# Performance work log

Hardware: AMD Instinct MI355X
Metric: run time of the kernel (lower is better)

## Reference

```python
import jax, jax.numpy as jnp
import numpy as np

B, L, IN, OUT = 32, 2048, 192, 2
H, N2, NL = 512, 32, 4  # hidden_dim, d_state//2 complex modes, num_layers


def setup_inputs() -> dict:
    key = jax.random.key(0)
    ks = jax.random.split(key, 8)
    neural_input = jax.random.normal(ks[0], (B, L, IN), jnp.float32)
    W_in = jax.random.normal(ks[1], (IN, H), jnp.float32) / np.sqrt(IN)
    b_in = jnp.zeros((H,), jnp.float32)
    # S4D kernel params (stacked over layers)
    log_dt = jax.random.uniform(ks[2], (NL, H), jnp.float32, np.log(1e-3), np.log(1e-1))
    Cri = jax.random.normal(ks[3], (NL, H, N2, 2), jnp.float32)  # complex C as (re, im)
    log_A_real = jnp.full((NL, H, N2), np.log(0.5), jnp.float32)
    A_imag = jnp.broadcast_to(np.pi * jnp.arange(N2, dtype=np.float32), (NL, H, N2)).astype(jnp.float32)
    D = jax.random.normal(ks[4], (NL, H), jnp.float32)
    # position-wise output conv1x1 producing 2H channels for GLU
    conv_w = jax.random.normal(ks[5], (NL, 2 * H, H), jnp.float32) / np.sqrt(H)
    conv_b = jnp.zeros((NL, 2 * H), jnp.float32)
    W_out = jax.random.normal(ks[6], (H, OUT), jnp.float32) / np.sqrt(H)
    b_out = jnp.zeros((OUT,), jnp.float32)
    return dict(neural_input=neural_input, W_in=W_in, b_in=b_in, log_dt=log_dt,
                Cri=Cri, log_A_real=log_A_real, A_imag=A_imag, D=D,
                conv_w=conv_w, conv_b=conv_b, W_out=W_out, b_out=b_out)


def _s4d_layer(u, log_dt, Cri, log_A_real, A_imag, D, conv_w, conv_b):
    # u: (B, H, L)
    Lx = u.shape[-1]
    dt = jnp.exp(log_dt)[:, None]                       # (H, 1)
    C = Cri[..., 0] + 1j * Cri[..., 1]                  # (H, N2) complex
    A = -jnp.exp(log_A_real) + 1j * A_imag              # (H, N2)
    dtA = A * dt                                        # (H, N2)
    Ct = C * (jnp.exp(dtA) - 1.0) / A                   # (H, N2)
    # Vandermonde kernel: K[h, l] = 2 Re sum_n Ct[h,n] exp(dtA[h,n] * l)
    vand = jnp.exp(dtA[..., None] * jnp.arange(Lx))     # (H, N2, L) complex
    K = 2.0 * jnp.einsum('hn,hnl->hl', Ct, vand).real   # (H, L)
    # circular conv via FFT at length 2L (== linear conv, causal)
    k_f = jnp.fft.rfft(K, n=2 * Lx)
    u_f = jnp.fft.rfft(u, n=2 * Lx)
    y = jnp.fft.irfft(u_f * k_f, n=2 * Lx)[..., :Lx]    # (B, H, L)
    y = y + u * D[:, None]
    y = jax.nn.gelu(y, approximate=False)               # torch nn.GELU (erf)
    # conv1x1 to 2H channels + GLU over channel dim
    z = jnp.einsum('oh,bhl->bol', conv_w, y) + conv_b[None, :, None]
    a, b = jnp.split(z, 2, axis=1)
    return a * jax.nn.sigmoid(b)


def reference(neural_input, W_in, b_in, log_dt, Cri, log_A_real, A_imag, D,
              conv_w, conv_b, W_out, b_out):
    x = neural_input @ W_in + b_in          # (B, L, H)
    u = jnp.transpose(x, (0, 2, 1))         # (B, H, L) channels-first for SSM
    for i in range(NL):
        u = _s4d_layer(u, log_dt[i], Cri[i], log_A_real[i], A_imag[i],
                       D[i], conv_w[i], conv_b[i])
    y = jnp.transpose(u, (0, 2, 1))         # (B, L, H)
    return y @ W_out + b_out                # (B, L, OUT)
```

## Files before the change

kernel.cpp:

```cpp
#include <hip/hip_runtime.h>
#include <hip/hip_bf16.h>
#include <math.h>

#define BB 32
#define LL 2048
#define INP 192
#define OUTC 2
#define HH 512
#define NN2 32
#define NNL 4
#define TABB 32768

using short8 = __attribute__((ext_vector_type(8))) short;
using f32x4  = __attribute__((ext_vector_type(4))) float;
using f32x2  = __attribute__((ext_vector_type(2))) float;

__device__ __forceinline__ float sigmoidf_(float x) {
  return 1.0f / (1.0f + expf(-x));
}
__device__ __forceinline__ unsigned short bf16bits(float x) {
  __hip_bfloat16 b = __float2bfloat16(x);
  return __builtin_bit_cast(unsigned short, b);
}
__device__ __forceinline__ float bfval(unsigned short b) {
  unsigned int u = (unsigned int)b << 16;
  return __builtin_bit_cast(float, u);
}
__device__ __forceinline__ float gelu_fast(float x) {
  float s = x * 0.70710678118654752f;
  float ax = fabsf(s);
  float tt = 1.0f / fmaf(0.3275911f, ax, 1.0f);
  float p = fmaf(1.061405429f, tt, -1.453152027f);
  p = fmaf(p, tt, 1.421413741f);
  p = fmaf(p, tt, -0.284496736f);
  p = fmaf(p, tt, 0.254829592f);
  float e = __expf(-s * s);
  float er = 1.0f - p * tt * e;
  er = copysignf(er, s);
  return 0.5f * x * (1.0f + er);
}
__device__ __forceinline__ void gload16(const void* gsrc, void* ldst) {
  __builtin_amdgcn_global_load_lds(
      (const __attribute__((address_space(1))) void*)gsrc,
      (__attribute__((address_space(3))) void*)ldst, 16, 0, 0);
}

__global__ __launch_bounds__(256) void k_params(const float* __restrict__ log_dt,
                                                const float* __restrict__ Cri,
                                                const float* __restrict__ lAr,
                                                const float* __restrict__ Aim,
                                                float* __restrict__ P) {
  int idx = blockIdx.x * 256 + threadIdx.x;
  if (idx >= NNL * HH * NN2) return;
  float dt  = expf(log_dt[idx / NN2]);
  float Are = -expf(lAr[idx]);
  float Aimv = Aim[idx];
  float dre = Are * dt, dim = Aimv * dt;
  float er = expf(dre);
  float wrv = er * cosf(dim);
  float wiv = er * sinf(dim);
  float Er = wrv - 1.0f, Ei = wiv;
  float den = Are * Are + Aimv * Aimv;
  float Fr = (Er * Are + Ei * Aimv) / den;
  float Fi = (Ei * Are - Er * Aimv) / den;
  float Cre = Cri[idx * 2 + 0], Cim = Cri[idx * 2 + 1];
  P[idx * 4 + 0] = wrv;
  P[idx * 4 + 1] = wiv;
  P[idx * 4 + 2] = 2.0f * (Cre * Fr - Cim * Fi);
  P[idx * 4 + 3] = 2.0f * (Cre * Fi + Cim * Fr);
}

__global__ __launch_bounds__(64) void k_tables(const float* __restrict__ P,
                                               char* __restrict__ Tab) {
  __shared__ float kk[32];
  int tid = threadIdx.x;
  int lh = blockIdx.x;
  char* tb = Tab + (size_t)lh * TABB;
  if (tid < 32) {
    int n = tid;
    const float4 pq = reinterpret_cast<const float4*>(P)[(size_t)lh * NN2 + n];
    float wr = pq.x, wi = pq.y, c2r = pq.z, c2i = pq.w;
    int mt = n >> 4;
    float pr = 1.0f, pi = 0.0f;
    for (int d = 0; d < 32; ++d) {
      {
        int t_ = 31 - d;
        int lane = ((t_ >> 3) << 4) + (n & 15);
        int j = t_ & 7;
        unsigned short hr = bf16bits(pr);
        unsigned short lr = bf16bits(pr - bfval(hr));
        unsigned short hi_ = bf16bits(pi);
        unsigned short li_ = bf16bits(pi - bfval(hi_));
        *(unsigned short*)(tb + (mt * 2 + 0) * 1024 + lane * 16 + j * 2) = hr;
        *(unsigned short*)(tb + (mt * 2 + 1) * 1024 + lane * 16 + j * 2) = hi_;
        *(unsigned short*)(tb + 4096 + (mt * 2 + 0) * 1024 + lane * 16 + j * 2) = lr;
        *(unsigned short*)(tb + 4096 + (mt * 2 + 1) * 1024 + lane * 16 + j * 2) = li_;
      }
      {
        int mtT = d >> 4;
        int lane = (((n & 15) >> 2) << 4) + (d & 15);
        int jre = n & 3, jim = (n & 3) + 4;
        unsigned short hr = bf16bits(pr);
        unsigned short lr = bf16bits(pr - bfval(hr));
        float nim = -pi;
        unsigned short hi_ = bf16bits(nim);
        unsigned short li_ = bf16bits(nim - bfval(hi_));
        char* bh = tb + 8192 + (mtT * 2 + mt) * 1024 + lane * 16;
        char* bl = tb + 12288 + (mtT * 2 + mt) * 1024 + lane * 16;
        *(unsigned short*)(bh + jre * 2) = hr;
        *(unsigned short*)(bh + jim * 2) = hi_;
        *(unsigned short*)(bl + jre * 2) = lr;
        *(unsigned short*)(bl + jim * 2) = li_;
      }
      float kp = c2r * pr - c2i * pi;
      #pragma unroll
      for (int k = 1; k < 32; k <<= 1) kp += __shfl_xor(kp, k, 32);
      if (n == 0) kk[d] = kp;
      float nr = pr * wr - pi * wi;
      pi = pr * wi + pi * wr;
      pr = nr;
    }
    float w32r = pr, w32i = pi;
    float c2wr = c2r * wr - c2i * wi;
    float c2wi = c2r * wi + c2i * wr;
    int s = ((n >> 4) << 2) + (n & 3);
    int gg = (n & 15) >> 2;
    float pmr = 1.0f, pmi = 0.0f;
    for (int m = 0; m < 16; ++m) {
      float* q = (float*)(tb + 20480 + (size_t)((s * 64) + (gg * 16 + m)) * 24);
      q[0] = w32r; q[1] = w32i; q[2] = pmr; q[3] = pmi; q[4] = c2wr; q[5] = c2wi;
      float t2 = pmr * w32r - pmi * w32i;
      pmi = pmr * w32i + pmi * w32r;
      pmr = t2;
    }
  }
  __syncthreads();
  for (int idx = tid; idx < 1024; idx += 64) {
    int mt = idx >> 9, rem = idx & 511;
    int lane = rem >> 3, j = rem & 7;
    int tt = (mt << 4) + (lane & 15);
    int jf = ((lane >> 4) << 3) + j;
    float val = (jf <= tt) ? kk[tt - jf] : 0.0f;
    unsigned short hb = bf16bits(val);
    unsigned short lb = bf16bits(val - bfval(hb));
    *(unsigned short*)(tb + 16384 + mt * 1024 + lane * 16 + j * 2) = hb;
    *(unsigned short*)(tb + 18432 + mt * 1024 + lane * 16 + j * 2) = lb;
  }
}

__global__ __launch_bounds__(256) void k_tobf16(const float* __restrict__ src,
                                                __hip_bfloat16* __restrict__ dst,
                                                int n) {
  int i = (blockIdx.x * 256 + threadIdx.x) * 4;
  if (i >= n) return;
  float4 v = *reinterpret_cast<const float4*>(&src[i]);
  dst[i + 0] = __float2bfloat16(v.x);
  dst[i + 1] = __float2bfloat16(v.y);
  dst[i + 2] = __float2bfloat16(v.z);
  dst[i + 3] = __float2bfloat16(v.w);
}

__global__ __launch_bounds__(256) void k_splitx(const float* __restrict__ src,
                                                __hip_bfloat16* __restrict__ hi,
                                                __hip_bfloat16* __restrict__ lo,
                                                int n) {
  int i = (blockIdx.x * 256 + threadIdx.x) * 4;
  if (i >= n) return;
  float4 v = *reinterpret_cast<const float4*>(&src[i]);
  float vv[4] = {v.x, v.y, v.z, v.w};
  unsigned short hb[4], lb[4];
  #pragma unroll
  for (int j = 0; j < 4; ++j) {
    hb[j] = bf16bits(vv[j]);
    lb[j] = bf16bits(vv[j] - bfval(hb[j]));
  }
  *reinterpret_cast<uint2*>(hi + i) = make_uint2(
      (unsigned)hb[0] | ((unsigned)hb[1] << 16), (unsigned)hb[2] | ((unsigned)hb[3] << 16));
  *reinterpret_cast<uint2*>(lo + i) = make_uint2(
      (unsigned)lb[0] | ((unsigned)lb[1] << 16), (unsigned)lb[2] | ((unsigned)lb[3] << 16));
}

__global__ __launch_bounds__(256) void k_prepwt(const float* __restrict__ W,
                                                __hip_bfloat16* __restrict__ hi,
                                                __hip_bfloat16* __restrict__ lo) {
  int idx = blockIdx.x * 256 + threadIdx.x;
  if (idx >= HH * INP) return;
  int h = idx / INP, k = idx - h * INP;
  float v = W[(size_t)k * HH + h];
  unsigned short hb = bf16bits(v);
  hi[idx] = __builtin_bit_cast(__hip_bfloat16, hb);
  lo[idx] = __float2bfloat16(v - bfval(hb));
}

__global__ __launch_bounds__(256) void k_ingemm(const __hip_bfloat16* __restrict__ Xhi,
                                                const __hip_bfloat16* __restrict__ Xlo,
                                                const __hip_bfloat16* __restrict__ Wthi,
                                                const __hip_bfloat16* __restrict__ Wtlo,
                                                const float* __restrict__ bias,
                                                float* __restrict__ U) {
  int lt = blockIdx.x * 128;
  int ht = blockIdx.y * 128;
  int b  = blockIdx.z;
  int t = threadIdx.x;
  int wid = t >> 6, lane = t & 63;
  int wrow = wid >> 1, wcol = wid & 1;
  int l15 = lane & 15, g = lane >> 4;

  const short* Xh = (const short*)Xhi + (size_t)b * LL * INP;
  const short* Xl = (const short*)Xlo + (size_t)b * LL * INP;
  const short* Bh = (const short*)Wthi;
  const short* Bl = (const short*)Wtlo;

  f32x4 acc[4][4];
  #pragma unroll
  for (int m = 0; m < 4; ++m)
    #pragma unroll
    for (int n = 0; n < 4; ++n) acc[m][n] = f32x4{0.f, 0.f, 0.f, 0.f};

  int lbase = lt + wrow * 64 + l15;
  int hbase = ht + wcol * 64 + l15;

  #pragma unroll
  for (int ks = 0; ks < 6; ++ks) {
    int k0 = ks * 32 + 8 * g;
    short8 ah[4], al[4], bh[4], bl[4];
    #pragma unroll
    for (int m = 0; m < 4; ++m) {
      size_t off = (size_t)(lbase + m * 16) * INP + k0;
      ah[m] = *reinterpret_cast<const short8*>(Xh + off);
      al[m] = *reinterpret_cast<const short8*>(Xl + off);
    }
    #pragma unroll
    for (int n = 0; n < 4; ++n) {
      size_t off = (size_t)(hbase + n * 16) * INP + k0;
      bh[n] = *reinterpret_cast<const short8*>(Bh + off);
      bl[n] = *reinterpret_cast<const short8*>(Bl + off);
    }
    #pragma unroll
    for (int m = 0; m < 4; ++m)
      #pragma unroll
      for (int n = 0; n < 4; ++n) {
        acc[m][n] = __builtin_amdgcn_mfma_f32_16x16x32_bf16(ah[m], bh[n], acc[m][n], 0, 0, 0);
        acc[m][n] = __builtin_amdgcn_mfma_f32_16x16x32_bf16(ah[m], bl[n], acc[m][n], 0, 0, 0);
        acc[m][n] = __builtin_amdgcn_mfma_f32_16x16x32_bf16(al[m], bh[n], acc[m][n], 0, 0, 0);
      }
  }

  #pragma unroll
  for (int n = 0; n < 4; ++n) {
    int h = hbase + n * 16;
    float bv = bias[h];
    #pragma unroll
    for (int m = 0; m < 4; ++m) {
      int l0 = lt + wrow * 64 + m * 16 + g * 4;
      float4 o;
      o.x = acc[m][n][0] + bv;
      o.y = acc[m][n][1] + bv;
      o.z = acc[m][n][2] + bv;
      o.w = acc[m][n][3] + bv;
      *reinterpret_cast<float4*>(&U[((size_t)b * HH + h) * LL + l0]) = o;
    }
  }
}

__global__ __launch_bounds__(256) void k_scan(const float* __restrict__ U,
                                              __hip_bfloat16* __restrict__ Ybf,
                                              const char* __restrict__ Tab,
                                              const float* __restrict__ Dp) {
  int t = threadIdx.x;
  int lane = t & 63;
  int row = __builtin_amdgcn_readfirstlane(blockIdx.x * 4 + (t >> 6));
  int h = row & (HH - 1);
  const char* tb = Tab + (size_t)h * TABB;
  const float* urow = U + (size_t)row * LL;
  int g = lane >> 4, m = lane & 15;

  short8 uh[4], ul[4];
  #pragma unroll
  for (int c0 = 0; c0 < 4; ++c0) {
    const float* p = urow + 512 * c0 + 32 * m + 8 * g;
    float4 va = *reinterpret_cast<const float4*>(p);
    float4 vb = *reinterpret_cast<const float4*>(p + 4);
    float v[8] = {va.x, va.y, va.z, va.w, vb.x, vb.y, vb.z, vb.w};
    short8 hi, lo;
    #pragma unroll
    for (int j = 0; j < 8; ++j) {
      unsigned short hb = bf16bits(v[j]);
      hi[j] = (short)hb;
      lo[j] = (short)bf16bits(v[j] - bfval(hb));
    }
    uh[c0] = hi;
    ul[c0] = lo;
  }

  f32x4 Z[2][2][4];
  #pragma unroll
  for (int mt = 0; mt < 2; ++mt)
    #pragma unroll
    for (int reim = 0; reim < 2; ++reim) {
      short8 whi = *reinterpret_cast<const short8*>(tb + (mt * 2 + reim) * 1024 + lane * 16);
      short8 wlo = *reinterpret_cast<const short8*>(tb + 4096 + (mt * 2 + reim) * 1024 + lane * 16);
      #pragma unroll
      for (int c0 = 0; c0 < 4; ++c0) {
        f32x4 z = {0.f, 0.f, 0.f, 0.f};
        z = __builtin_amdgcn_mfma_f32_16x16x32_bf16(whi, uh[c0], z, 0, 0, 0);
        z = __builtin_amdgcn_mfma_f32_16x16x32_bf16(whi, ul[c0], z, 0, 0, 0);
        z = __builtin_amdgcn_mfma_f32_16x16x32_bf16(wlo, uh[c0], z, 0, 0, 0);
        Z[mt][reim][c0] = z;
      }
    }

  float aR[8][4], aI[8][4];
  #pragma unroll
  for (int s = 0; s < 8; ++s) {
    int mt = s >> 2, i = s & 3;
    const char* plb = tb + 20480 + (size_t)(s * 64 + lane) * 24;
    f32x2 w32 = *reinterpret_cast<const f32x2*>(plb);
    f32x2 w32m = *reinterpret_cast<const f32x2*>(plb + 8);
    f32x2 c2w = *reinterpret_cast<const f32x2*>(plb + 16);
    float r1r = w32[0], r1i = w32[1];
    float r2r = r1r * r1r - r1i * r1i, r2i = 2.f * r1r * r1i;
    float r4r = r2r * r2r - r2i * r2i, r4i = 2.f * r2r * r2i;
    float r8r = r4r * r4r - r4i * r4i, r8i = 2.f * r4r * r4i;
    float w16r = r8r * r8r - r8i * r8i, w16i = 2.f * r8r * r8i;
    float Sr = 0.f, Si = 0.f;
    #pragma unroll
    for (int c0 = 0; c0 < 4; ++c0) {
      float Pr = Z[mt][0][c0][i], Pi = Z[mt][1][c0][i];
      {
        float qr = __shfl_up(Pr, 1u, 16), qi = __shfl_up(Pi, 1u, 16);
        if (m < 1) { qr = 0.f; qi = 0.f; }
        Pr = fmaf(r1r, qr, fmaf(-r1i, qi, Pr));
        Pi = fmaf(r1r, qi, fmaf(r1i, qr, Pi));
      }
      {
        float qr = __shfl_up(Pr, 2u, 16), qi = __shfl_up(Pi, 2u, 16);
        if (m < 2) { qr = 0.f; qi = 0.f; }
        Pr = fmaf(r2r, qr, fmaf(-r2i, qi, Pr));
        Pi = fmaf(r2r, qi, fmaf(r2i, qr, Pi));
      }
      {
        float qr = __shfl_up(Pr, 4u, 16), qi = __shfl_up(Pi, 4u, 16);
        if (m < 4) { qr = 0.f; qi = 0.f; }
        Pr = fmaf(r4r, qr, fmaf(-r4i, qi, Pr));
        Pi = fmaf(r4r, qi, fmaf(r4i, qr, Pi));
      }
      {
        float qr = __shfl_up(Pr, 8u, 16), qi = __shfl_up(Pi, 8u, 16);
        if (m < 8) { qr = 0.f; qi = 0.f; }
        Pr = fmaf(r8r, qr, fmaf(-r8i, qi, Pr));
        Pi = fmaf(r8r, qi, fmaf(r8i, qr, Pi));
      }
      float eqr = __shfl_up(Pr, 1u, 16), eqi = __shfl_up(Pi, 1u, 16);
      if (m == 0) { eqr = 0.f; eqi = 0.f; }
      float Er = fmaf(w32m[0], Sr, fmaf(-w32m[1], Si, eqr));
      float Ei = fmaf(w32m[0], Si, fmaf(w32m[1], Sr, eqi));
      aR[s][c0] = c2w[0] * Er - c2w[1] * Ei;
      aI[s][c0] = c2w[0] * Ei + c2w[1] * Er;
      float lr = __shfl(Pr, 15, 16), li = __shfl(Pi, 15, 16);
      float nS = fmaf(w16r, Sr, fmaf(-w16i, Si, lr));
      Si = fmaf(w16r, Si, fmaf(w16i, Sr, li));
      Sr = nS;
    }
  }

  short8 afh[2][4], afl[2][4];
  #pragma unroll
  for (int kt = 0; kt < 2; ++kt)
    #pragma unroll
    for (int c0 = 0; c0 < 4; ++c0) {
      float av[8] = {aR[kt * 4 + 0][c0], aR[kt * 4 + 1][c0], aR[kt * 4 + 2][c0], aR[kt * 4 + 3][c0],
                     aI[kt * 4 + 0][c0], aI[kt * 4 + 1][c0], aI[kt * 4 + 2][c0], aI[kt * 4 + 3][c0]};
      short8 hi, lo;
      #pragma unroll
      for (int j = 0; j < 8; ++j) {
        unsigned short hb = bf16bits(av[j]);
        hi[j] = (short)hb;
        lo[j] = (short)bf16bits(av[j] - bfval(hb));
      }
      afh[kt][c0] = hi;
      afl[kt][c0] = lo;
    }

  f32x4 y[2][4];
  #pragma unroll
  for (int mtT = 0; mtT < 2; ++mtT) {
    short8 fh = *reinterpret_cast<const short8*>(tb + 16384 + mtT * 1024 + lane * 16);
    short8 fl = *reinterpret_cast<const short8*>(tb + 18432 + mtT * 1024 + lane * 16);
    short8 wch0 = *reinterpret_cast<const short8*>(tb + 8192 + (mtT * 2 + 0) * 1024 + lane * 16);
    short8 wcl0 = *reinterpret_cast<const short8*>(tb + 12288 + (mtT * 2 + 0) * 1024 + lane * 16);
    short8 wch1 = *reinterpret_cast<const short8*>(tb + 8192 + (mtT * 2 + 1) * 1024 + lane * 16);
    short8 wcl1 = *reinterpret_cast<const short8*>(tb + 12288 + (mtT * 2 + 1) * 1024 + lane * 16);
    #pragma unroll
    for (int c0 = 0; c0 < 4; ++c0) {
      f32x4 acc = {0.f, 0.f, 0.f, 0.f};
      acc = __builtin_amdgcn_mfma_f32_16x16x32_bf16(fh, uh[c0], acc, 0, 0, 0);
      acc = __builtin_amdgcn_mfma_f32_16x16x32_bf16(fh, ul[c0], acc, 0, 0, 0);
      acc = __builtin_amdgcn_mfma_f32_16x16x32_bf16(fl, uh[c0], acc, 0, 0, 0);
      acc = __builtin_amdgcn_mfma_f32_16x16x32_bf16(wch0, afh[0][c0], acc, 0, 0, 0);
      acc = __builtin_amdgcn_mfma_f32_16x16x32_bf16(wch0, afl[0][c0], acc, 0, 0, 0);
      acc = __builtin_amdgcn_mfma_f32_16x16x32_bf16(wcl0, afh[0][c0], acc, 0, 0, 0);
      acc = __builtin_amdgcn_mfma_f32_16x16x32_bf16(wch1, afh[1][c0], acc, 0, 0, 0);
      acc = __builtin_amdgcn_mfma_f32_16x16x32_bf16(wch1, afl[1][c0], acc, 0, 0, 0);
      acc = __builtin_amdgcn_mfma_f32_16x16x32_bf16(wcl1, afh[1][c0], acc, 0, 0, 0);
      y[mtT][c0] = acc;
    }
  }

  float Dv = Dp[h];
  #pragma unroll
  for (int mtT = 0; mtT < 2; ++mtT)
    #pragma unroll
    for (int c0 = 0; c0 < 4; ++c0) {
      int eb = 512 * c0 + 32 * m + 16 * mtT + 4 * g;
      float4 uu = *reinterpret_cast<const float4*>(urow + eb);
      f32x4 vv = y[mtT][c0];
      unsigned short b0 = bf16bits(gelu_fast(fmaf(Dv, uu.x, vv[0])));
      unsigned short b1 = bf16bits(gelu_fast(fmaf(Dv, uu.y, vv[1])));
      unsigned short b2 = bf16bits(gelu_fast(fmaf(Dv, uu.z, vv[2])));
      unsigned short b3 = bf16bits(gelu_fast(fmaf(Dv, uu.w, vv[3])));
      uint2 wo;
      wo.x = (unsigned int)b0 | ((unsigned int)b1 << 16);
      wo.y = (unsigned int)b2 | ((unsigned int)b3 << 16);
      *reinterpret_cast<uint2*>(Ybf + (size_t)row * LL + eb) = wo;
    }
}

__global__ __launch_bounds__(256) void k_transpose(const __hip_bfloat16* __restrict__ src,
                                                   __hip_bfloat16* __restrict__ dst) {
  __shared__ short lds[32][132];
  int t = threadIdx.x;
  int l0 = blockIdx.x * 128;
  int h0 = blockIdx.y * 32;
  int b  = blockIdx.z;
  const short* S = (const short*)(src + (size_t)b * HH * LL);
  short* D = (short*)(dst + (size_t)b * LL * HH);
  {
    int h = t >> 3, s0 = (t & 7) * 2;
    #pragma unroll
    for (int s = s0; s < s0 + 2; ++s) {
      float4 v = *reinterpret_cast<const float4*>(&S[(size_t)(h0 + h) * LL + l0 + s * 8]);
      *reinterpret_cast<float2*>(&lds[h][s * 8])     = make_float2(v.x, v.y);
      *reinterpret_cast<float2*>(&lds[h][s * 8 + 4]) = make_float2(v.z, v.w);
    }
  }
  __syncthreads();
  {
    int l = t >> 1, half = t & 1;
    unsigned int w[8];
    #pragma unroll
    for (int j = 0; j < 8; ++j) {
      unsigned short s0 = (unsigned short)lds[half * 16 + 2 * j][l];
      unsigned short s1 = (unsigned short)lds[half * 16 + 2 * j + 1][l];
      w[j] = (unsigned int)s0 | ((unsigned int)s1 << 16);
    }
    uint4* dp = reinterpret_cast<uint4*>(&D[(size_t)(l0 + l) * HH + h0 + half * 16]);
    dp[0] = make_uint4(w[0], w[1], w[2], w[3]);
    dp[1] = make_uint4(w[4], w[5], w[6], w[7]);
  }
}

__global__ __launch_bounds__(256) void k_conv(const __hip_bfloat16* __restrict__ Ytb,
                                              const __hip_bfloat16* __restrict__ CWb,
                                              const float* __restrict__ CB,
                                              float* __restrict__ U) {
  __shared__ short Alds[128 * 64];
  __shared__ short Blds[128 * 64];
  int lt = blockIdx.x * 128;
  int ot = blockIdx.y * 64;
  int b  = blockIdx.z;
  int t = threadIdx.x;
  int wid = t >> 6, lane = t & 63;
  int wr = wid >> 1, wc = wid & 1;
  int l15 = lane & 15, l4 = lane >> 4;
  f32x4 zero = {0.f, 0.f, 0.f, 0.f};
  f32x4 accA[2][4], accG[2][4];
  #pragma unroll
  for (int m = 0; m < 2; ++m)
    #pragma unroll
    for (int n = 0; n < 4; ++n) { accA[m][n] = zero; accG[m][n] = zero; }

  const char* Yb = (const char*)(Ytb + (size_t)b * LL * HH);
  const char* Wb = (const char*)CWb;

  for (int kt = 0; kt < HH; kt += 64) {
    #pragma unroll
    for (int it = 0; it < 4; ++it) {
      int d = 16 * (t + 256 * it);
      int rowl = d >> 7, cb = d & 127;
      int orow = (rowl < 64) ? (ot + rowl) : (448 + ot + rowl);
      gload16(Wb + (size_t)orow * 1024 + kt * 2 + (cb ^ ((rowl & 7) << 4)),
              (char*)Alds + d);
    }
    #pragma unroll
    for (int it = 0; it < 4; ++it) {
      int d = 16 * (t + 256 * it);
      int rowl = d >> 7, cb = d & 127;
      gload16(Yb + ((size_t)(lt + rowl) * 512 + kt) * 2 + (cb ^ ((rowl & 7) << 4)),
              (char*)Blds + d);
    }
    __syncthreads();
    #pragma unroll
    for (int ks = 0; ks < 2; ++ks) {
      short8 af[4], bf[4];
      #pragma unroll
      for (int m = 0; m < 4; ++m) {
        int mrow = ((m < 2) ? (wr * 32 + m * 16) : (64 + wr * 32 + (m - 2) * 16)) + l15;
        int colb = (ks * 64 + 16 * l4) ^ ((mrow & 7) << 4);
        af[m] = *reinterpret_cast<const short8*>((const char*)Alds + mrow * 128 + colb);
      }
      #pragma unroll
      for (int n = 0; n < 4; ++n) {
        int nrow = wc * 64 + n * 16 + l15;
        int colb = (ks * 64 + 16 * l4) ^ ((nrow & 7) << 4);
        bf[n] = *reinterpret_cast<const short8*>((const char*)Blds + nrow * 128 + colb);
      }
      #pragma unroll
      for (int m = 0; m < 2; ++m)
        #pragma unroll
        for (int n = 0; n < 4; ++n) {
          accA[m][n] = __builtin_amdgcn_mfma_f32_16x16x32_bf16(af[m], bf[n], accA[m][n], 0, 0, 0);
          accG[m][n] = __builtin_amdgcn_mfma_f32_16x16x32_bf16(af[m + 2], bf[n], accG[m][n], 0, 0, 0);
        }
    }
    __syncthreads();
  }
  #pragma unroll
  for (int m = 0; m < 2; ++m) {
    #pragma unroll
    for (int r = 0; r < 4; ++r) {
      int rowl = wr * 32 + m * 16 + l4 * 4 + r;
      float ba = CB[ot + rowl];
      float bg = CB[512 + ot + rowl];
      float* urow_ = U + ((size_t)b * HH + ot + rowl) * LL + lt + wc * 64;
      #pragma unroll
      for (int n = 0; n < 4; ++n) {
        float a = accA[m][n][r] + ba;
        float g = accG[m][n][r] + bg;
        urow_[n * 16 + l15] = a * sigmoidf_(g);
      }
    }
  }
}

__global__ __launch_bounds__(256) void k_outgemm(const float* __restrict__ U,
                                                 const float* __restrict__ Wo,
                                                 const float* __restrict__ bo,
                                                 float* __restrict__ out) {
  int bl = blockIdx.x * 256 + threadIdx.x;
  int b = bl >> 11, l = bl & (LL - 1);
  float a0 = 0.0f, a1 = 0.0f;
  const float* up = U + (size_t)b * HH * LL + l;
  #pragma unroll 4
  for (int h = 0; h < HH; ++h) {
    float v = up[(size_t)h * LL];
    a0 = fmaf(v, Wo[h * 2 + 0], a0);
    a1 = fmaf(v, Wo[h * 2 + 1], a1);
  }
  out[(size_t)bl * 2 + 0] = a0 + bo[0];
  out[(size_t)bl * 2 + 1] = a1 + bo[1];
}

extern "C" void kernel_launch(void* const* d_in, const int* in_sizes, int n_in,
                              void* d_out, int out_size, void* d_ws, size_t ws_size,
                              hipStream_t stream) {
  const float* X      = (const float*)d_in[0];
  const float* Win    = (const float*)d_in[1];
  const float* bin    = (const float*)d_in[2];
  const float* log_dt = (const float*)d_in[3];
  const float* Cri    = (const float*)d_in[4];
  const float* lAr    = (const float*)d_in[5];
  const float* Aim    = (const float*)d_in[6];
  const float* Dp     = (const float*)d_in[7];
  const float* CW     = (const float*)d_in[8];
  const float* CB     = (const float*)d_in[9];
  const float* Wo     = (const float*)d_in[10];
  const float* bo     = (const float*)d_in[11];
  float* out = (float*)d_out;

  const size_t Pfloats   = (size_t)NNL * HH * NN2 * 4;
  const size_t CWfloats  = (size_t)NNL * 2 * HH * HH / 2;
  const size_t Tabfloats = (size_t)NNL * HH * (TABB / 4);
  const size_t Wtfloats  = (size_t)HH * INP;
  const size_t Xnf       = (size_t)BB * LL * INP;
  const size_t HL        = (size_t)HH * LL;

  float* P = (float*)d_ws;
  __hip_bfloat16* CWb = (__hip_bfloat16*)(P + Pfloats);
  char* Tab = (char*)(P + Pfloats + CWfloats);
  __hip_bfloat16* Wthi = (__hip_bfloat16*)(P + Pfloats + CWfloats + Tabfloats);
  __hip_bfloat16* Wtlo = Wthi + Wtfloats;
  __hip_bfloat16* Xhi  = (__hip_bfloat16*)(P + Pfloats + CWfloats + Tabfloats + Wtfloats);
  __hip_bfloat16* Xlo  = Xhi + Xnf;
  size_t head = Pfloats + CWfloats + Tabfloats + Wtfloats + Xnf;

  size_t ws_floats = ws_size / sizeof(float);
  size_t avail = (ws_floats > head) ? (ws_floats - head) : 0;
  int G = (int)(avail / (HL + HL / 2));
  if (G >= 32) G = 32;
  else if (G >= 16) G = 16;
  else if (G >= 8) G = 8;
  else if (G >= 4) G = 4;
  else if (G >= 2) G = 2;
  else G = 1;

  float* U = P + head;
  __hip_bfloat16* Ybf = (__hip_bfloat16*)(U + (size_t)G * HL);
  __hip_bfloat16* Yt  = Ybf + (size_t)G * HL;

  k_params<<<(NNL * HH * NN2 + 255) / 256, 256, 0, stream>>>(log_dt, Cri, lAr, Aim, P);
  k_tables<<<NNL * HH, 64, 0, stream>>>(P, Tab);
  k_tobf16<<<(NNL * 2 * HH * HH) / 1024, 256, 0, stream>>>(CW, CWb, NNL * 2 * HH * HH);
  k_prepwt<<<(HH * INP + 255) / 256, 256, 0, stream>>>(Win, Wthi, Wtlo);
  k_splitx<<<(int)(Xnf / 1024), 256, 0, stream>>>(X, Xhi, Xlo, (int)Xnf);

  for (int b0 = 0; b0 < BB; b0 += G) {
    int g = (BB - b0 < G) ? (BB - b0) : G;
    k_ingemm<<<dim3(LL / 128, HH / 128, g), 256, 0, stream>>>(
        Xhi + (size_t)b0 * LL * INP, Xlo + (size_t)b0 * LL * INP, Wthi, Wtlo, bin, U);
    for (int layer = 0; layer < NNL; ++layer) {
      k_scan<<<g * (HH / 4), 256, 0, stream>>>(
          U, Ybf,
          Tab + (size_t)layer * HH * TABB,
          Dp + (size_t)layer * HH);
      k_transpose<<<dim3(LL / 128, HH / 32, g), 256, 0, stream>>>(Ybf, Yt);
      k_conv<<<dim3(LL / 128, HH / 64, g), 256, 0, stream>>>(
          Yt, CWb + (size_t)layer * 2 * HH * HH, CB + (size_t)layer * 2 * HH, U);
    }
    k_outgemm<<<g * LL / 256, 256, 0, stream>>>(
        U, Wo, bo, out + (size_t)b0 * LL * OUTC);
  }
}
```

Baseline: 1.290 ms.

## Fuse transpose into scan epilogue via blocked layout read directly by conv

The scan kernel now processes 8 channels per block, stages its GELU bf16 outputs in shared memory, and writes them in a blocked layout of 8 channels × L. The conv kernel loads its B fragments straight from global memory in that layout instead of staging them through LDS. This removes the separate transpose kernel and its extra global round trip of activations per layer. The cost is larger scan blocks with 32KB of LDS and un-staged global B loads in conv, which may be less coalesced or less well overlapped.

```diff
diff --git a/kernel.cpp b/kernel.cpp
--- a/kernel.cpp
+++ b/kernel.cpp
@@ -263,13 +263,15 @@
   }
 }
 
-__global__ __launch_bounds__(256) void k_scan(const float* __restrict__ U,
-                                              __hip_bfloat16* __restrict__ Ybf,
+__global__ __launch_bounds__(512) void k_scan(const float* __restrict__ U,
+                                              short* __restrict__ Ybt,
                                               const char* __restrict__ Tab,
                                               const float* __restrict__ Dp) {
+  __shared__ short ylds[8 * 2048];
   int t = threadIdx.x;
   int lane = t & 63;
-  int row = __builtin_amdgcn_readfirstlane(blockIdx.x * 4 + (t >> 6));
+  int wid = t >> 6;
+  int row = __builtin_amdgcn_readfirstlane(blockIdx.x * 8 + wid);
   int h = row & (HH - 1);
   const char* tb = Tab + (size_t)h * TABB;
   const float* urow = U + (size_t)row * LL;
@@ -415,57 +417,32 @@
       int eb = 512 * c0 + 32 * m + 16 * mtT + 4 * g;
       float4 uu = *reinterpret_cast<const float4*>(urow + eb);
       f32x4 vv = y[mtT][c0];
-      unsigned short b0 = bf16bits(gelu_fast(fmaf(Dv, uu.x, vv[0])));
-      unsigned short b1 = bf16bits(gelu_fast(fmaf(Dv, uu.y, vv[1])));
-      unsigned short b2 = bf16bits(gelu_fast(fmaf(Dv, uu.z, vv[2])));
-      unsigned short b3 = bf16bits(gelu_fast(fmaf(Dv, uu.w, vv[3])));
-      uint2 wo;
-      wo.x = (unsigned int)b0 | ((unsigned int)b1 << 16);
-      wo.y = (unsigned int)b2 | ((unsigned int)b3 << 16);
-      *reinterpret_cast<uint2*>(Ybf + (size_t)row * LL + eb) = wo;
-    }
-}
-
-__global__ __launch_bounds__(256) void k_transpose(const __hip_bfloat16* __restrict__ src,
-                                                   __hip_bfloat16* __restrict__ dst) {
-  __shared__ short lds[32][132];
-  int t = threadIdx.x;
-  int l0 = blockIdx.x * 128;
-  int h0 = blockIdx.y * 32;
-  int b  = blockIdx.z;
-  const short* S = (const short*)(src + (size_t)b * HH * LL);
-  short* D = (short*)(dst + (size_t)b * LL * HH);
-  {
-    int h = t >> 3, s0 = (t & 7) * 2;
-    #pragma unroll
-    for (int s = s0; s < s0 + 2; ++s) {
-      float4 v = *reinterpret_cast<const float4*>(&S[(size_t)(h0 + h) * LL + l0 + s * 8]);
-      *reinterpret_cast<float2*>(&lds[h][s * 8])     = make_float2(v.x, v.y);
-      *reinterpret_cast<float2*>(&lds[h][s * 8 + 4]) = make_float2(v.z, v.w);
-    }
-  }
+      unsigned short bv[4];
+      bv[0] = bf16bits(gelu_fast(fmaf(Dv, uu.x, vv[0])));
+      bv[1] = bf16bits(gelu_fast(fmaf(Dv, uu.y, vv[1])));
+      bv[2] = bf16bits(gelu_fast(fmaf(Dv, uu.z, vv[2])));
+      bv[3] = bf16bits(gelu_fast(fmaf(Dv, uu.w, vv[3])));
+      int ymask = ((eb >> 5) & 7) << 4;
+      #pragma unroll
+      for (int k = 0; k < 4; ++k) {
+        *(short*)((char*)ylds + (((eb + k) * 16 + wid * 2) ^ ymask)) = (short)bv[k];
+      }
+    }
   __syncthreads();
-  {
-    int l = t >> 1, half = t & 1;
-    unsigned int w[8];
-    #pragma unroll
-    for (int j = 0; j < 8; ++j) {
-      unsigned short s0 = (unsigned short)lds[half * 16 + 2 * j][l];
-      unsigned short s1 = (unsigned short)lds[half * 16 + 2 * j + 1][l];
-      w[j] = (unsigned int)s0 | ((unsigned int)s1 << 16);
-    }
-    uint4* dp = reinterpret_cast<uint4*>(&D[(size_t)(l0 + l) * HH + h0 + half * 16]);
-    dp[0] = make_uint4(w[0], w[1], w[2], w[3]);
-    dp[1] = make_uint4(w[4], w[5], w[6], w[7]);
-  }
-}
-
-__global__ __launch_bounds__(256) void k_conv(const __hip_bfloat16* __restrict__ Ytb,
+  #pragma unroll
+  for (int i = 0; i < 4; ++i) {
+    int l = t + 512 * i;
+    int ymask = ((l >> 5) & 7) << 4;
+    uint4 v = *reinterpret_cast<const uint4*>((const char*)ylds + ((l * 16) ^ ymask));
+    *reinterpret_cast<uint4*>(Ybt + ((size_t)blockIdx.x * 2048 + l) * 8) = v;
+  }
+}
+
+__global__ __launch_bounds__(256) void k_conv(const short* __restrict__ Ybt,
                                               const __hip_bfloat16* __restrict__ CWb,
                                               const float* __restrict__ CB,
                                               float* __restrict__ U) {
   __shared__ short Alds[128 * 64];
-  __shared__ short Blds[128 * 64];
   int lt = blockIdx.x * 128;
   int ot = blockIdx.y * 64;
   int b  = blockIdx.z;
@@ -480,7 +457,7 @@
     #pragma unroll
     for (int n = 0; n < 4; ++n) { accA[m][n] = zero; accG[m][n] = zero; }
 
-  const char* Yb = (const char*)(Ytb + (size_t)b * LL * HH);
+  const short* Yb = Ybt + (size_t)b * 64 * 2048 * 8;
   const char* Wb = (const char*)CWb;
 
   for (int kt = 0; kt < HH; kt += 64) {
@@ -492,17 +469,20 @@
       gload16(Wb + (size_t)orow * 1024 + kt * 2 + (cb ^ ((rowl & 7) << 4)),
               (char*)Alds + d);
     }
-    #pragma unroll
-    for (int it = 0; it < 4; ++it) {
-      int d = 16 * (t + 256 * it);
-      int rowl = d >> 7, cb = d & 127;
-      gload16(Yb + ((size_t)(lt + rowl) * 512 + kt) * 2 + (cb ^ ((rowl & 7) << 4)),
-              (char*)Blds + d);
-    }
+    short8 bfrag[2][4];
+    #pragma unroll
+    for (int ks = 0; ks < 2; ++ks)
+      #pragma unroll
+      for (int n = 0; n < 4; ++n) {
+        int l = lt + wc * 64 + n * 16 + l15;
+        int octg = (kt >> 3) + ks * 4 + l4;
+        bfrag[ks][n] = *reinterpret_cast<const short8*>(
+            Yb + ((size_t)octg * 2048 + l) * 8);
+      }
     __syncthreads();
     #pragma unroll
     for (int ks = 0; ks < 2; ++ks) {
-      short8 af[4], bf[4];
+      short8 af[4];
       #pragma unroll
       for (int m = 0; m < 4; ++m) {
         int mrow = ((m < 2) ? (wr * 32 + m * 16) : (64 + wr * 32 + (m - 2) * 16)) + l15;
@@ -510,17 +490,11 @@
         af[m] = *reinterpret_cast<const short8*>((const char*)Alds + mrow * 128 + colb);
       }
       #pragma unroll
-      for (int n = 0; n < 4; ++n) {
-        int nrow = wc * 64 + n * 16 + l15;
-        int colb = (ks * 64 + 16 * l4) ^ ((nrow & 7) << 4);
-        bf[n] = *reinterpret_cast<const short8*>((const char*)Blds + nrow * 128 + colb);
-      }
-      #pragma unroll
       for (int m = 0; m < 2; ++m)
         #pragma unroll
         for (int n = 0; n < 4; ++n) {
-          accA[m][n] = __builtin_amdgcn_mfma_f32_16x16x32_bf16(af[m], bf[n], accA[m][n], 0, 0, 0);
-          accG[m][n] = __builtin_amdgcn_mfma_f32_16x16x32_bf16(af[m + 2], bf[n], accG[m][n], 0, 0, 0);
+          accA[m][n] = __builtin_amdgcn_mfma_f32_16x16x32_bf16(af[m], bfrag[ks][n], accA[m][n], 0, 0, 0);
+          accG[m][n] = __builtin_amdgcn_mfma_f32_16x16x32_bf16(af[m + 2], bfrag[ks][n], accG[m][n], 0, 0, 0);
         }
     }
     __syncthreads();
@@ -605,8 +579,7 @@
   else G = 1;
 
   float* U = P + head;
-  __hip_bfloat16* Ybf = (__hip_bfloat16*)(U + (size_t)G * HL);
-  __hip_bfloat16* Yt  = Ybf + (size_t)G * HL;
+  short* Ybt = (short*)(U + (size_t)G * HL);
 
   k_params<<<(NNL * HH * NN2 + 255) / 256, 256, 0, stream>>>(log_dt, Cri, lAr, Aim, P);
   k_tables<<<NNL * HH, 64, 0, stream>>>(P, Tab);
@@ -619,13 +592,12 @@
     k_ingemm<<<dim3(LL / 128, HH / 128, g), 256, 0, stream>>>(
         Xhi + (size_t)b0 * LL * INP, Xlo + (size_t)b0 * LL * INP, Wthi, Wtlo, bin, U);
     for (int layer = 0; layer < NNL; ++layer) {
-      k_scan<<<g * (HH / 4), 256, 0, stream>>>(
-          U, Ybf,
+      k_scan<<<g * (HH / 8), 512, 0, stream>>>(
+          U, Ybt,
           Tab + (size_t)layer * HH * TABB,
           Dp + (size_t)layer * HH);
-      k_transpose<<<dim3(LL / 128, HH / 32, g), 256, 0, stream>>>(Ybf, Yt);
       k_conv<<<dim3(LL / 128, HH / 64, g), 256, 0, stream>>>(
-          Yt, CWb + (size_t)layer * 2 * HH * HH, CB + (size_t)layer * 2 * HH, U);
+          Ybt, CWb + (size_t)layer * 2 * HH * HH, CB + (size_t)layer * 2 * HH, U);
     }
     k_outgemm<<<g * LL / 256, 256, 0, stream>>>(
         U, Wo, bo, out + (size_t)b0 * LL * OUTC);
```

Result: faster. 1.236 ms (-4.1%).
